# Kernel tuning notes

Measured on AMD Instinct MI355X. Metric: run time of the kernel, lower is better.

## Reference

```python
import jax, jax.numpy as jnp
import numpy as np

EPS = 1e-5

def conv1d(x, w, b):
    # Keras Conv1D, channels_last, padding='same'. x: [B,L,Cin], w: [K,Cin,Cout]
    y = jax.lax.conv_general_dilated(x, w, window_strides=(1,), padding='SAME',
                                     dimension_numbers=('NWC', 'WIO', 'NWC'))
    return y + b

def rmsnorm(x, w):
    return x * jax.lax.rsqrt(jnp.mean(jnp.square(x), axis=-1, keepdims=True) + EPS) * w

def setup_inputs() -> dict:
    key = jax.random.key(0)
    ks = jax.random.split(key, 12)
    B, L, D, S = 4, 4096, 512, 16
    D2 = 2 * D
    def w(k, shape, scale=0.02):
        return (jax.random.normal(k, shape, jnp.float32) * scale)
    return {
        'x': jax.random.normal(ks[0], (B, L, D), jnp.float32),
        'norm_w': jnp.ones((D,), jnp.float32),
        'inp_w': w(ks[1], (3, D, D2)),  'inp_b': jnp.zeros((D2,), jnp.float32),
        'conv_w': w(ks[2], (3, D2, D2)), 'conv_b': jnp.zeros((D2,), jnp.float32),
        'cl_w': w(ks[3], (3, D2, D2)),   'cl_b': jnp.zeros((D2,), jnp.float32),
        'fc1_w': w(ks[4], (3, D2, D2)),  'fc1_b': jnp.zeros((D2,), jnp.float32),
        'fc2_w': w(ks[5], (3, D2, S)),   'fc2_b': jnp.zeros((S,), jnp.float32),
        'fc3_w': w(ks[6], (3, D2, S)),   'fc3_b': jnp.zeros((S,), jnp.float32),
        'A': w(ks[7], (D2, S), 0.1),
        'res_w': w(ks[8], (3, D, D2)),   'res_b': jnp.zeros((D2,), jnp.float32),
        'out_w': w(ks[9], (3, D2, D)),   'out_b': jnpp if False else jnp.zeros((D,), jnp.float32),
    }

def s6(x, fc1_w, fc1_b, fc2_w, fc2_b, fc3_w, fc3_b, A):
    # Original: dB = delta[...,None]*B[:,:,None,:]; dA = exp(delta[...,None]*A);
    # h = dA * zeros + x[...,None] * dB  ==  x[...,None] * dB  (dA term is exactly 0)
    # y = einsum('bln,bldn->bld', C, h) = x * delta * sum_n(C*B)
    Bm = conv1d(x, fc2_w, fc2_b)            # [B,L,n]
    Cm = conv1d(x, fc3_w, fc3_b)            # [B,L,n]
    delta = jax.nn.softplus(conv1d(x, fc1_w, fc1_b))  # [B,L,2d]
    cb = jnp.einsum('bln,bln->bl', Cm, Bm)  # [B,L]
    return x * delta * cb[..., None]        # [B,L,2d]

def reference(x, norm_w, inp_w, inp_b, conv_w, conv_b, cl_w, cl_b,
              fc1_w, fc1_b, fc2_w, fc2_b, fc3_w, fc3_b, A,
              res_w, res_b, out_w, out_b):
    xn = rmsnorm(x, norm_w)
    x_proj = conv1d(xn, inp_w, inp_b)
    x_conv = jax.nn.swish(conv1d(x_proj, conv_w, conv_b))
    x_conv_out = conv1d(x_conv, cl_w, cl_b)
    x_ssm = s6(x_conv_out, fc1_w, fc1_b, fc2_w, fc2_b, fc3_w, fc3_b, A)
    x_res = jax.nn.swish(conv1d(xn, res_w, res_b))
    return conv1d(x_ssm * x_res, out_w, out_b)
```

## Files before the change

kernel.cpp:

```cpp
#include <hip/hip_runtime.h>
#include <hip/hip_fp16.h>

typedef _Float16 f16;
typedef _Float16 half8  __attribute__((ext_vector_type(8)));
typedef _Float16 half4v __attribute__((ext_vector_type(4)));
typedef _Float16 half2v __attribute__((ext_vector_type(2)));
typedef float    floatx4 __attribute__((ext_vector_type(4)));

constexpr int SEQ  = 4096;
constexpr int SEQP = 4098;

__device__ __forceinline__ void dma16(const void* g, char* ldsBase, unsigned off) {
  __builtin_amdgcn_global_load_lds(
      (const __attribute__((address_space(1))) void*)g,
      (__attribute__((address_space(3))) void*)(ldsBase + off),
      16, 0, 0);
}

template <int EPI>
__global__ __launch_bounds__(256, 2)
void gemm_k(const f16* __restrict__ A, const f16* __restrict__ Wt,
            const float* __restrict__ bias, void* __restrict__ Cp,
            void* __restrict__ Cp2,
            int kSlice, int lda, long bsA, int ldb,
            int ldc, long bsC, int rowOff)
{
  __shared__ f16 lds[16384];
  char* ldsB = (char*)lds;

  const int tid  = threadIdx.x;
  const int lane = tid & 63;
  const int wv   = tid >> 6;
  const int quad = lane >> 4;
  const int lr   = lane & 15;
  const int w_row = wv >> 1, w_col = wv & 1;

  const int r0 = blockIdx.x * 128;
  const int n0 = blockIdx.y * 128;
  const int b  = r0 >> 12;
  const int l0 = r0 & (SEQ - 1);
  const int kBeg = blockIdx.z * kSlice;

  const int trow   = tid >> 3;
  const int tchunk = ((tid & 7) ^ ((tid >> 3) & 7)) * 8;
  const f16* gA = A + (long)b * bsA + (long)(l0 + trow) * lda + kBeg + tchunk;
  const f16* gB = Wt + (long)(n0 + trow) * ldb + kBeg + tchunk;
  const long stepA = 32l * lda, stepB = 32l * ldb;

  floatx4 acc[4][4];
#pragma unroll
  for (int mi = 0; mi < 4; mi++)
#pragma unroll
    for (int ni = 0; ni < 4; ni++) acc[mi][ni] = (floatx4){0.f, 0.f, 0.f, 0.f};

  const int colx = (quad ^ (lr & 7)) * 8;

  for (int k0 = 0; k0 < kSlice; k0 += 64) {
    __syncthreads();
#pragma unroll
    for (int j = 0; j < 4; j++) {
      dma16(gA + k0 + j * stepA, ldsB,         j * 4096 + wv * 1024);
      dma16(gB + k0 + j * stepB, ldsB, 16384 + j * 4096 + wv * 1024);
    }
    __syncthreads();

#pragma unroll
    for (int s = 0; s < 2; s++) {
      const int cs = colx ^ (s * 32);
      half8 af[4], bf[4];
#pragma unroll
      for (int mi = 0; mi < 4; mi++)
        af[mi] = *(const half8*)&lds[(w_row * 64 + mi * 16 + lr) * 64 + cs];
#pragma unroll
      for (int ni = 0; ni < 4; ni++)
        bf[ni] = *(const half8*)&lds[8192 + (w_col * 64 + ni * 16 + lr) * 64 + cs];
#pragma unroll
      for (int mi = 0; mi < 4; mi++)
#pragma unroll
        for (int ni = 0; ni < 4; ni++)
          acc[mi][ni] = __builtin_amdgcn_mfma_f32_16x16x32_f16(af[mi], bf[ni], acc[mi][ni], 0, 0, 0);
    }
  }

  const int colBase = n0 + w_col * 64 + lr;
  float bv[4];
#pragma unroll
  for (int ni = 0; ni < 4; ni++)
    bv[ni] = (EPI == 6 && blockIdx.z != 0) ? 0.f : bias[colBase + ni * 16];

  const long cbb = (long)b * bsC;
#pragma unroll
  for (int mi = 0; mi < 4; mi++) {
#pragma unroll
    for (int i = 0; i < 4; i++) {
      const int rl = w_row * 64 + mi * 16 + quad * 4 + i;
      const long rowFlat = cbb + (long)(l0 + rl + rowOff) * ldc;
      const int rg = r0 + rl;
#pragma unroll
      for (int ni = 0; ni < 4; ni++) {
        const int c = colBase + ni * 16;
        float v = acc[mi][ni][i] + bv[ni];
        if (EPI == 0) {
          ((f16*)Cp)[rowFlat + c] = (f16)v;
        } else if (EPI == 1) {
          v = v / (1.f + expf(-v));
          ((f16*)Cp)[rowFlat + c] = (f16)v;
        } else if (EPI == 2) {
          ((float*)Cp)[rowFlat + c] = v;
        } else if (EPI == 5) {
          if (c < 1024) {
            ((f16*)Cp)[cbb + (long)(l0 + rl + 1) * 1024 + c] = (f16)v;
          } else {
            v = v / (1.f + expf(-v));
            ((f16*)Cp2)[(long)rg * 1024 + (c - 1024)] = (f16)v;
          }
        } else {
          if (c < 32) atomicAdd((float*)Cp + (long)rg * 32 + c, v);
        }
      }
    }
  }
}

__global__ __launch_bounds__(256)
void wt_all(const float* __restrict__ s0, const float* __restrict__ s1,
            const float* __restrict__ s2, const float* __restrict__ s3,
            const float* __restrict__ s4, const float* __restrict__ s5,
            f16* d0, f16* d1, f16* d2, f16* d3, f16* d4, f16* d5)
{
  const float* src; f16* dst; int K, N;
  switch (blockIdx.y) {
    case 0:  src = s0; dst = d0; K = 1536; N = 1024; break;
    case 1:  src = s1; dst = d1; K = 3072; N = 1024; break;
    case 2:  src = s2; dst = d2; K = 3072; N = 1024; break;
    case 3:  src = s3; dst = d3; K = 3072; N = 1024; break;
    case 4:  src = s4; dst = d4; K = 1536; N = 1024; break;
    default: src = s5; dst = d5; K = 3072; N = 512;  break;
  }
  const int ktiles = K >> 5;
  const int t = blockIdx.x;
  if (t >= ktiles * (N >> 5)) return;
  const int kt = (t % ktiles) * 32, nt = (t / ktiles) * 32;

  __shared__ float tile[32][33];
  const int tx = threadIdx.x & 31, ty = threadIdx.x >> 5;
#pragma unroll
  for (int i = 0; i < 32; i += 8)
    tile[ty + i][tx] = src[(long)(kt + ty + i) * N + nt + tx];
  __syncthreads();
#pragma unroll
  for (int i = 0; i < 32; i += 8)
    dst[(long)(nt + ty + i) * K + kt + tx] = (f16)tile[tx][ty + i];
}

__global__ void fc23_build(const float* __restrict__ fc2, const float* __restrict__ fc3,
                           f16* __restrict__ wt)
{
  int idx = blockIdx.x * 256 + threadIdx.x;
  int n = idx / 3072, k = idx - n * 3072;
  float v = 0.f;
  if (n < 16)      v = fc2[k * 16 + n];
  else if (n < 32) v = fc3[k * 16 + n - 16];
  wt[idx] = (f16)v;
}

__global__ void bias_build(const float* __restrict__ bi, const float* __restrict__ br,
                           const float* __restrict__ b2, const float* __restrict__ b3,
                           float* __restrict__ b_inpres, float* __restrict__ b_fc23)
{
  int t = blockIdx.x * 256 + threadIdx.x;
  if (t < 1024)      b_inpres[t] = bi[t];
  else if (t < 2048) b_inpres[t] = br[t - 1024];
  else if (t < 2176) {
    int u = t - 2048;
    b_fc23[u] = u < 16 ? b2[u] : (u < 32 ? b3[u - 16] : 0.f);
  }
}

__global__ void zero_pads(f16* xn, f16* xproj, f16* xconv, f16* xco)
{
  int b = blockIdx.x >> 1, e = blockIdx.x & 1;
  f16* base; int C;
  switch (blockIdx.y) {
    case 0:  base = xn;    C = 512;  break;
    case 1:  base = xproj; C = 1024; break;
    case 2:  base = xconv; C = 1024; break;
    default: base = xco;   C = 1024; break;
  }
  long p = e ? (SEQP - 1) : 0;
  f16* row = base + ((long)b * SEQP + p) * C;
  for (int c = threadIdx.x; c < C; c += 256) row[c] = (f16)0;
}

__global__ void zero_f32(float4* p)
{
  p[blockIdx.x * 256 + threadIdx.x] = (float4){0.f, 0.f, 0.f, 0.f};
}

__global__ __launch_bounds__(256)
void rmsnorm_k(const float* __restrict__ x, const float* __restrict__ nw,
               f16* __restrict__ xn)
{
  const int row = blockIdx.x;
  const int b = row >> 12, l = row & (SEQ - 1);
  const int t = threadIdx.x;
  float2 v = ((const float2*)(x + (long)row * 512))[t];
  float ss = v.x * v.x + v.y * v.y;
#pragma unroll
  for (int o = 32; o > 0; o >>= 1) ss += __shfl_down(ss, o, 64);
  __shared__ float sred[4];
  if ((t & 63) == 0) sred[t >> 6] = ss;
  __syncthreads();
  float tot = sred[0] + sred[1] + sred[2] + sred[3];
  float rs = rsqrtf(tot * (1.f / 512.f) + 1e-5f);
  float2 w = ((const float2*)nw)[t];
  half2v o2;
  o2.x = (f16)(v.x * rs * w.x);
  o2.y = (f16)(v.y * rs * w.y);
  ((half2v*)(xn + ((long)b * SEQP + l + 1) * 512))[t] = o2;
}

__global__ __launch_bounds__(256)
void combine_k(const f16* __restrict__ delta_pre, const f16* __restrict__ xco_pad,
               const float* __restrict__ bmcmF, const f16* __restrict__ xres,
               f16* __restrict__ prod_pad)
{
  const int row = blockIdx.x;
  const int b = row >> 12, l = row & (SEQ - 1);
  const int t = threadIdx.x;
  __shared__ float cb_s;
  if (t < 16) {
    float p = bmcmF[(long)row * 32 + t] * bmcmF[(long)row * 32 + 16 + t];
#pragma unroll
    for (int o = 8; o > 0; o >>= 1) p += __shfl_down(p, o, 64);
    if (t == 0) cb_s = p;
  }
  __syncthreads();
  const float cb = cb_s;
  const long urow = (long)row * 1024;
  const long prow = ((long)b * SEQP + l + 1) * 1024;
  half4v dp = ((const half4v*)(delta_pre + urow))[t];
  half4v xc = ((const half4v*)(xco_pad + prow))[t];
  half4v xr = ((const half4v*)(xres + urow))[t];
  half4v o;
#pragma unroll
  for (int j = 0; j < 4; j++) {
    float d  = (float)dp[j];
    float sp = d > 20.f ? d : log1pf(expf(d));
    o[j] = (f16)((float)xc[j] * sp * cb * (float)xr[j]);
  }
  ((half4v*)(prod_pad + prow))[t] = o;
}

extern "C" void kernel_launch(void* const* d_in, const int* in_sizes, int n_in,
                              void* d_out, int out_size, void* d_ws, size_t ws_size,
                              hipStream_t stream)
{
  const float* x      = (const float*)d_in[0];
  const float* norm_w = (const float*)d_in[1];
  const float* inp_w  = (const float*)d_in[2];
  const float* inp_b  = (const float*)d_in[3];
  const float* conv_w = (const float*)d_in[4];
  const float* conv_b = (const float*)d_in[5];
  const float* cl_w   = (const float*)d_in[6];
  const float* cl_b   = (const float*)d_in[7];
  const float* fc1_w  = (const float*)d_in[8];
  const float* fc1_b  = (const float*)d_in[9];
  const float* fc2_w  = (const float*)d_in[10];
  const float* fc2_b  = (const float*)d_in[11];
  const float* fc3_w  = (const float*)d_in[12];
  const float* fc3_b  = (const float*)d_in[13];
  const float* res_w  = (const float*)d_in[15];
  const float* res_b  = (const float*)d_in[16];
  const float* out_w  = (const float*)d_in[17];
  const float* out_b  = (const float*)d_in[18];

  char* ws = (char*)d_ws;
  size_t off = 0;
  auto alloc = [&](size_t bytes) -> char* {
    char* p = ws + off; off += (bytes + 511) & ~(size_t)511; return p;
  };
  f16* Wt_inpres = (f16*)alloc(2048ull * 1536 * 2);
  f16* Wt_conv   = (f16*)alloc(1024ull * 3072 * 2);
  f16* Wt_cl     = (f16*)alloc(1024ull * 3072 * 2);
  f16* Wt_fc1    = (f16*)alloc(1024ull * 3072 * 2);
  f16* Wt_fc23   = (f16*)alloc(128ull  * 3072 * 2);
  f16* Wt_out    = (f16*)alloc(512ull  * 3072 * 2);
  float* b_inpres = (float*)alloc(2048 * 4);
  float* b_fc23   = (float*)alloc(128 * 4);
  f16* xn_pad    = (f16*)alloc(4ull * SEQP * 512  * 2);
  f16* xproj_pad = (f16*)alloc(4ull * SEQP * 1024 * 2);
  f16* xconv_pad = (f16*)alloc(4ull * SEQP * 1024 * 2);
  f16* xco_pad   = (f16*)alloc(4ull * SEQP * 1024 * 2);
  f16* xres      = (f16*)alloc(16384ull * 1024 * 2);
  float* bmcmF   = (float*)alloc(16384ull * 32 * 4);

  wt_all<<<dim3(3072, 6), 256, 0, stream>>>(inp_w, conv_w, cl_w, fc1_w, res_w, out_w,
      Wt_inpres, Wt_conv, Wt_cl, Wt_fc1, Wt_inpres + 1024ull * 1536, Wt_out);
  fc23_build<<<1536, 256, 0, stream>>>(fc2_w, fc3_w, Wt_fc23);
  bias_build<<<9, 256, 0, stream>>>(inp_b, res_b, fc2_b, fc3_b, b_inpres, b_fc23);
  zero_pads<<<dim3(8, 4), 256, 0, stream>>>(xn_pad, xproj_pad, xconv_pad, xco_pad);
  zero_f32<<<512, 256, 0, stream>>>((float4*)bmcmF);

  rmsnorm_k<<<16384, 256, 0, stream>>>(x, norm_w, xn_pad);

  gemm_k<5><<<dim3(128, 16), 256, 0, stream>>>(xn_pad, Wt_inpres, b_inpres,
      xproj_pad, xres, 1536, 512, (long)SEQP * 512, 1536, 1024, (long)SEQP * 1024, 1);
  gemm_k<1><<<dim3(128, 8), 256, 0, stream>>>(xproj_pad, Wt_conv, conv_b,
      xconv_pad, nullptr, 3072, 1024, (long)SEQP * 1024, 3072, 1024, (long)SEQP * 1024, 1);
  gemm_k<0><<<dim3(128, 8), 256, 0, stream>>>(xconv_pad, Wt_cl, cl_b,
      xco_pad, nullptr, 3072, 1024, (long)SEQP * 1024, 3072, 1024, (long)SEQP * 1024, 1);
  f16* delta_pre = xconv_pad;
  gemm_k<0><<<dim3(128, 8), 256, 0, stream>>>(xco_pad, Wt_fc1, fc1_b,
      delta_pre, nullptr, 3072, 1024, (long)SEQP * 1024, 3072, 1024, (long)SEQ * 1024, 0);
  gemm_k<6><<<dim3(128, 1, 8), 256, 0, stream>>>(xco_pad, Wt_fc23, b_fc23,
      bmcmF, nullptr, 384, 1024, (long)SEQP * 1024, 3072, 32, (long)SEQ * 32, 0);
  f16* prod_pad = xproj_pad;
  combine_k<<<16384, 256, 0, stream>>>(delta_pre, xco_pad, bmcmF, xres, prod_pad);
  gemm_k<2><<<dim3(128, 4), 256, 0, stream>>>(prod_pad, Wt_out, out_b,
      d_out, nullptr, 3072, 1024, (long)SEQP * 1024, 3072, 512, (long)SEQ * 512, 0);
}
```

Baseline: 723.9 us.

## Fuse softplus/combine into fc1 GEMM epilogue, merge prep kernels, swap grid order

The fc1 GEMM now computes softplus in its epilogue and multiplies by the conv output, the residual branch and a precomputed per-row C·B scalar, writing the product directly. This removes the delta_pre round trip and the separate combine kernel. A small cb_k kernel computes the per-row dot product beforehand. Several small setup kernels are merged into wt_all and misc_prep to cut launches. The grid is transposed so blocks that share a weight tile run together, which may change L2 reuse. The epilogue's scattered reads of A and xres per element could be uncoalesced.

```diff
diff --git a/kernel.cpp b/kernel.cpp
--- a/kernel.cpp
+++ b/kernel.cpp
@@ -21,7 +21,7 @@
 __global__ __launch_bounds__(256, 2)
 void gemm_k(const f16* __restrict__ A, const f16* __restrict__ Wt,
             const float* __restrict__ bias, void* __restrict__ Cp,
-            void* __restrict__ Cp2,
+            void* __restrict__ Cp2, const float* __restrict__ Ecb,
             int kSlice, int lda, long bsA, int ldb,
             int ldc, long bsC, int rowOff)
 {
@@ -35,8 +35,8 @@
   const int lr   = lane & 15;
   const int w_row = wv >> 1, w_col = wv & 1;
 
-  const int r0 = blockIdx.x * 128;
-  const int n0 = blockIdx.y * 128;
+  const int n0 = blockIdx.x * 128;
+  const int r0 = blockIdx.y * 128;
   const int b  = r0 >> 12;
   const int l0 = r0 & (SEQ - 1);
   const int kBeg = blockIdx.z * kSlice;
@@ -114,8 +114,13 @@
             v = v / (1.f + expf(-v));
             ((f16*)Cp2)[(long)rg * 1024 + (c - 1024)] = (f16)v;
           }
+        } else if (EPI == 6) {
+          if (c < 32) atomicAdd((float*)Cp + (long)rg * 32 + c, v);
         } else {
-          if (c < 32) atomicAdd((float*)Cp + (long)rg * 32 + c, v);
+          float sp = v > 20.f ? v : log1pf(expf(v));
+          float xc = (float)A[rowFlat + c];
+          float xr = (float)((const f16*)Cp2)[(long)rg * 1024 + c];
+          ((f16*)Cp)[rowFlat + c] = (f16)(xc * sp * Ecb[rg] * xr);
         }
       }
     }
@@ -126,8 +131,24 @@
 void wt_all(const float* __restrict__ s0, const float* __restrict__ s1,
             const float* __restrict__ s2, const float* __restrict__ s3,
             const float* __restrict__ s4, const float* __restrict__ s5,
-            f16* d0, f16* d1, f16* d2, f16* d3, f16* d4, f16* d5)
-{
+            const float* __restrict__ fc2, const float* __restrict__ fc3,
+            f16* d0, f16* d1, f16* d2, f16* d3, f16* d4, f16* d5, f16* d6)
+{
+  if (blockIdx.y == 6) {
+    const int t = blockIdx.x;
+    if (t >= 384) return;
+    const int n = t / 3, k0 = (t % 3) * 1024 + threadIdx.x * 4;
+    half4v o;
+#pragma unroll
+    for (int j = 0; j < 4; j++) {
+      float v = 0.f;
+      if (n < 16)      v = fc2[(k0 + j) * 16 + n];
+      else if (n < 32) v = fc3[(k0 + j) * 16 + n - 16];
+      o[j] = (f16)v;
+    }
+    *(half4v*)(d6 + (long)n * 3072 + k0) = o;
+    return;
+  }
   const float* src; f16* dst; int K, N;
   switch (blockIdx.y) {
     case 0:  src = s0; dst = d0; K = 1536; N = 1024; break;
@@ -153,48 +174,36 @@
     dst[(long)(nt + ty + i) * K + kt + tx] = (f16)tile[tx][ty + i];
 }
 
-__global__ void fc23_build(const float* __restrict__ fc2, const float* __restrict__ fc3,
-                           f16* __restrict__ wt)
-{
-  int idx = blockIdx.x * 256 + threadIdx.x;
-  int n = idx / 3072, k = idx - n * 3072;
-  float v = 0.f;
-  if (n < 16)      v = fc2[k * 16 + n];
-  else if (n < 32) v = fc3[k * 16 + n - 16];
-  wt[idx] = (f16)v;
-}
-
-__global__ void bias_build(const float* __restrict__ bi, const float* __restrict__ br,
-                           const float* __restrict__ b2, const float* __restrict__ b3,
-                           float* __restrict__ b_inpres, float* __restrict__ b_fc23)
-{
-  int t = blockIdx.x * 256 + threadIdx.x;
-  if (t < 1024)      b_inpres[t] = bi[t];
-  else if (t < 2048) b_inpres[t] = br[t - 1024];
-  else if (t < 2176) {
-    int u = t - 2048;
-    b_fc23[u] = u < 16 ? b2[u] : (u < 32 ? b3[u - 16] : 0.f);
-  }
-}
-
-__global__ void zero_pads(f16* xn, f16* xproj, f16* xconv, f16* xco)
-{
-  int b = blockIdx.x >> 1, e = blockIdx.x & 1;
-  f16* base; int C;
-  switch (blockIdx.y) {
-    case 0:  base = xn;    C = 512;  break;
-    case 1:  base = xproj; C = 1024; break;
-    case 2:  base = xconv; C = 1024; break;
-    default: base = xco;   C = 1024; break;
-  }
-  long p = e ? (SEQP - 1) : 0;
-  f16* row = base + ((long)b * SEQP + p) * C;
-  for (int c = threadIdx.x; c < C; c += 256) row[c] = (f16)0;
-}
-
-__global__ void zero_f32(float4* p)
-{
-  p[blockIdx.x * 256 + threadIdx.x] = (float4){0.f, 0.f, 0.f, 0.f};
+__global__ __launch_bounds__(256)
+void misc_prep(const float* __restrict__ bi, const float* __restrict__ br,
+               const float* __restrict__ b2, const float* __restrict__ b3,
+               float* __restrict__ b_inpres, float* __restrict__ b_fc23,
+               float* __restrict__ bmcmF,
+               f16* xn, f16* xproj, f16* xconv, f16* xco)
+{
+  const int bid = blockIdx.x, tid = threadIdx.x;
+  if (bid < 512) {
+    ((float4*)bmcmF)[bid * 256 + tid] = (float4){0.f, 0.f, 0.f, 0.f};
+  } else if (bid < 521) {
+    int t = (bid - 512) * 256 + tid;
+    if (t < 1024)      b_inpres[t] = bi[t];
+    else if (t < 2048) b_inpres[t] = br[t - 1024];
+    else if (t < 2176) {
+      int u = t - 2048;
+      b_fc23[u] = u < 16 ? b2[u] : (u < 32 ? b3[u - 16] : 0.f);
+    }
+  } else {
+    int u = (bid - 521) * 256 + tid;
+    if (u >= 3584) return;
+    int grp = u / 448, rem = u - grp * 448;
+    int b = grp >> 1, e = grp & 1;
+    long p = e ? (SEQP - 1) : 0;
+    float4 z = (float4){0.f, 0.f, 0.f, 0.f};
+    if (rem < 64)       ((float4*)(xn    + ((long)b * SEQP + p) * 512 ))[rem]       = z;
+    else if (rem < 192) ((float4*)(xproj + ((long)b * SEQP + p) * 1024))[rem - 64]  = z;
+    else if (rem < 320) ((float4*)(xconv + ((long)b * SEQP + p) * 1024))[rem - 192] = z;
+    else                ((float4*)(xco   + ((long)b * SEQP + p) * 1024))[rem - 320] = z;
+  }
 }
 
 __global__ __launch_bounds__(256)
@@ -221,35 +230,16 @@
 }
 
 __global__ __launch_bounds__(256)
-void combine_k(const f16* __restrict__ delta_pre, const f16* __restrict__ xco_pad,
-               const float* __restrict__ bmcmF, const f16* __restrict__ xres,
-               f16* __restrict__ prod_pad)
-{
-  const int row = blockIdx.x;
-  const int b = row >> 12, l = row & (SEQ - 1);
-  const int t = threadIdx.x;
-  __shared__ float cb_s;
-  if (t < 16) {
-    float p = bmcmF[(long)row * 32 + t] * bmcmF[(long)row * 32 + 16 + t];
-#pragma unroll
-    for (int o = 8; o > 0; o >>= 1) p += __shfl_down(p, o, 64);
-    if (t == 0) cb_s = p;
-  }
-  __syncthreads();
-  const float cb = cb_s;
-  const long urow = (long)row * 1024;
-  const long prow = ((long)b * SEQP + l + 1) * 1024;
-  half4v dp = ((const half4v*)(delta_pre + urow))[t];
-  half4v xc = ((const half4v*)(xco_pad + prow))[t];
-  half4v xr = ((const half4v*)(xres + urow))[t];
-  half4v o;
-#pragma unroll
-  for (int j = 0; j < 4; j++) {
-    float d  = (float)dp[j];
-    float sp = d > 20.f ? d : log1pf(expf(d));
-    o[j] = (f16)((float)xc[j] * sp * cb * (float)xr[j]);
-  }
-  ((half4v*)(prod_pad + prow))[t] = o;
+void cb_k(const float* __restrict__ bmcmF, float* __restrict__ cb)
+{
+  int r = blockIdx.x * 256 + threadIdx.x;
+  const float4* p = (const float4*)(bmcmF + (long)r * 32);
+  float4 q0 = p[0], q1 = p[1], q2 = p[2], q3 = p[3];
+  float4 q4 = p[4], q5 = p[5], q6 = p[6], q7 = p[7];
+  cb[r] = q0.x*q4.x + q0.y*q4.y + q0.z*q4.z + q0.w*q4.w
+        + q1.x*q5.x + q1.y*q5.y + q1.z*q5.z + q1.w*q5.w
+        + q2.x*q6.x + q2.y*q6.y + q2.z*q6.z + q2.w*q6.w
+        + q3.x*q7.x + q3.y*q7.y + q3.z*q7.z + q3.w*q7.w;
 }
 
 extern "C" void kernel_launch(void* const* d_in, const int* in_sizes, int n_in,
@@ -294,29 +284,34 @@
   f16* xco_pad   = (f16*)alloc(4ull * SEQP * 1024 * 2);
   f16* xres      = (f16*)alloc(16384ull * 1024 * 2);
   float* bmcmF   = (float*)alloc(16384ull * 32 * 4);
-
-  wt_all<<<dim3(3072, 6), 256, 0, stream>>>(inp_w, conv_w, cl_w, fc1_w, res_w, out_w,
-      Wt_inpres, Wt_conv, Wt_cl, Wt_fc1, Wt_inpres + 1024ull * 1536, Wt_out);
-  fc23_build<<<1536, 256, 0, stream>>>(fc2_w, fc3_w, Wt_fc23);
-  bias_build<<<9, 256, 0, stream>>>(inp_b, res_b, fc2_b, fc3_b, b_inpres, b_fc23);
-  zero_pads<<<dim3(8, 4), 256, 0, stream>>>(xn_pad, xproj_pad, xconv_pad, xco_pad);
-  zero_f32<<<512, 256, 0, stream>>>((float4*)bmcmF);
+  float* cb      = (float*)alloc(16384ull * 4);
+
+  wt_all<<<dim3(3072, 7), 256, 0, stream>>>(inp_w, conv_w, cl_w, fc1_w, res_w, out_w,
+      fc2_w, fc3_w,
+      Wt_inpres, Wt_conv, Wt_cl, Wt_fc1, Wt_inpres + 1024ull * 1536, Wt_out, Wt_fc23);
+  misc_prep<<<535, 256, 0, stream>>>(inp_b, res_b, fc2_b, fc3_b,
+      b_inpres, b_fc23, bmcmF, xn_pad, xproj_pad, xconv_pad, xco_pad);
 
   rmsnorm_k<<<16384, 256, 0, stream>>>(x, norm_w, xn_pad);
 
-  gemm_k<5><<<dim3(128, 16), 256, 0, stream>>>(xn_pad, Wt_inpres, b_inpres,
-      xproj_pad, xres, 1536, 512, (long)SEQP * 512, 1536, 1024, (long)SEQP * 1024, 1);
-  gemm_k<1><<<dim3(128, 8), 256, 0, stream>>>(xproj_pad, Wt_conv, conv_b,
-      xconv_pad, nullptr, 3072, 1024, (long)SEQP * 1024, 3072, 1024, (long)SEQP * 1024, 1);
-  gemm_k<0><<<dim3(128, 8), 256, 0, stream>>>(xconv_pad, Wt_cl, cl_b,
-      xco_pad, nullptr, 3072, 1024, (long)SEQP * 1024, 3072, 1024, (long)SEQP * 1024, 1);
-  f16* delta_pre = xconv_pad;
-  gemm_k<0><<<dim3(128, 8), 256, 0, stream>>>(xco_pad, Wt_fc1, fc1_b,
-      delta_pre, nullptr, 3072, 1024, (long)SEQP * 1024, 3072, 1024, (long)SEQ * 1024, 0);
-  gemm_k<6><<<dim3(128, 1, 8), 256, 0, stream>>>(xco_pad, Wt_fc23, b_fc23,
-      bmcmF, nullptr, 384, 1024, (long)SEQP * 1024, 3072, 32, (long)SEQ * 32, 0);
+  gemm_k<5><<<dim3(16, 128), 256, 0, stream>>>(xn_pad, Wt_inpres, b_inpres,
+      xproj_pad, xres, nullptr,
+      1536, 512, (long)SEQP * 512, 1536, 1024, (long)SEQP * 1024, 1);
+  gemm_k<1><<<dim3(8, 128), 256, 0, stream>>>(xproj_pad, Wt_conv, conv_b,
+      xconv_pad, nullptr, nullptr,
+      3072, 1024, (long)SEQP * 1024, 3072, 1024, (long)SEQP * 1024, 1);
+  gemm_k<0><<<dim3(8, 128), 256, 0, stream>>>(xconv_pad, Wt_cl, cl_b,
+      xco_pad, nullptr, nullptr,
+      3072, 1024, (long)SEQP * 1024, 3072, 1024, (long)SEQP * 1024, 1);
+  gemm_k<6><<<dim3(1, 128, 8), 256, 0, stream>>>(xco_pad, Wt_fc23, b_fc23,
+      bmcmF, nullptr, nullptr,
+      384, 1024, (long)SEQP * 1024, 3072, 32, (long)SEQ * 32, 0);
+  cb_k<<<64, 256, 0, stream>>>(bmcmF, cb);
   f16* prod_pad = xproj_pad;
-  combine_k<<<16384, 256, 0, stream>>>(delta_pre, xco_pad, bmcmF, xres, prod_pad);
-  gemm_k<2><<<dim3(128, 4), 256, 0, stream>>>(prod_pad, Wt_out, out_b,
-      d_out, nullptr, 3072, 1024, (long)SEQP * 1024, 3072, 512, (long)SEQ * 512, 0);
-}
+  gemm_k<7><<<dim3(8, 128), 256, 0, stream>>>(xco_pad, Wt_fc1, fc1_b,
+      prod_pad, xres, cb,
+      3072, 1024, (long)SEQP * 1024, 3072, 1024, (long)SEQP * 1024, 1);
+  gemm_k<2><<<dim3(4, 128), 256, 0, stream>>>(prod_pad, Wt_out, out_b,
+      d_out, nullptr, nullptr,
+      3072, 1024, (long)SEQP * 1024, 3072, 512, (long)SEQ * 512, 0);
+}
```

New measurement: 794.7 us. 1.1x slower.
